# Kernel optimization log

Hardware: AMD Instinct MI355X
Metric: run time of the kernel (lower is better)

Reference implementation:

```python
import jax, jax.numpy as jnp
import numpy as np

N = 50000
E = 800000
D = 256   # output_channel_dim
K = 32
L = 4     # num_of_layers


def setup_inputs() -> dict:
    key = jax.random.key(0)
    ks = jax.random.split(key, 10)
    x = jax.random.normal(ks[0], (N, 1), dtype=jnp.float32)
    edge_index = jax.random.randint(ks[1], (2, E), 0, N, dtype=jnp.int64)
    edge_attr = jax.random.uniform(ks[2], (E,), dtype=jnp.float32)
    # GGNN per-layer propagation weights (L, D, D)
    weight = jax.random.normal(ks[3], (L, D, D), dtype=jnp.float32) / np.sqrt(D)
    # GRUCell params (torch layout: [r|z|n] stacked along first dim)
    w_ih = jax.random.normal(ks[4], (3 * D, D), dtype=jnp.float32) / np.sqrt(D)
    w_hh = jax.random.normal(ks[5], (3 * D, D), dtype=jnp.float32) / np.sqrt(D)
    b_ih = jax.random.normal(ks[6], (3 * D,), dtype=jnp.float32) * 0.01
    b_hh = jax.random.normal(ks[7], (3 * D,), dtype=jnp.float32) * 0.01
    # readout Linear(D, K)
    w_ro = jax.random.normal(ks[8], (D, K), dtype=jnp.float32) / np.sqrt(D)
    b_ro = jax.random.normal(ks[9], (K,), dtype=jnp.float32) * 0.01
    return {"x": x, "edge_index": edge_index, "edge_attr": edge_attr,
            "weight": weight, "w_ih": w_ih, "w_hh": w_hh,
            "b_ih": b_ih, "b_hh": b_hh, "w_ro": w_ro, "b_ro": b_ro}


def _gru_cell(m, h, w_ih, w_hh, b_ih, b_hh):
    # torch.nn.GRUCell math; gates stacked [r|z|n]
    gi = m @ w_ih.T + b_ih   # (N, 3D)
    gh = h @ w_hh.T + b_hh   # (N, 3D)
    i_r, i_z, i_n = jnp.split(gi, 3, axis=-1)
    h_r, h_z, h_n = jnp.split(gh, 3, axis=-1)
    r = jax.nn.sigmoid(i_r + h_r)
    z = jax.nn.sigmoid(i_z + h_z)
    n = jnp.tanh(i_n + r * h_n)
    return (1.0 - z) * n + z * h


def reference(x, edge_index, edge_attr, weight, w_ih, w_hh, b_ih, b_hh, w_ro, b_ro):
    src, dst = edge_index[0], edge_index[1]
    n_nodes, d = x.shape[0], weight.shape[-1]
    # pad input features with zeros up to out_channels
    h = jnp.concatenate([x, jnp.zeros((n_nodes, d - x.shape[-1]), x.dtype)], axis=-1)
    for i in range(weight.shape[0]):
        m = h @ weight[i]                                    # (N, D)
        msg = edge_attr[:, None] * m[src]                    # (E, D)
        agg = jax.ops.segment_sum(msg, dst, num_segments=n_nodes)  # (N, D)
        h = _gru_cell(agg, h, w_ih, w_hh, b_ih, b_hh)
    logits = h @ w_ro + b_ro                                 # (N, K)
    return jax.nn.softmax(logits, axis=-1)
```

## Files before the change

kernel.cpp:

```cpp
#include <hip/hip_runtime.h>

#define D 256
#define K_OUT 32
#define L_LAYERS 4
#define NPAD 50048

typedef __attribute__((ext_vector_type(8))) short bf16x8;
typedef __attribute__((ext_vector_type(4))) float f32x4;
typedef __attribute__((address_space(3))) unsigned int lds_u32;
typedef const __attribute__((address_space(1))) unsigned int glb_u32;

__device__ __forceinline__ float sigm(float v) { return 1.f / (1.f + __expf(-v)); }
__device__ __forceinline__ unsigned short f2bf(float f) {
    unsigned u = __float_as_uint(f);
    u = u + 0x7fffu + ((u >> 16) & 1u);
    return (unsigned short)(u >> 16);
}
__device__ __forceinline__ float bf2f(unsigned short s) {
    return __uint_as_float(((unsigned)s) << 16);
}
__device__ __forceinline__ void gload16(const unsigned short* g, unsigned short* l) {
    __builtin_amdgcn_global_load_lds((glb_u32*)g, (lds_u32*)l, 16, 0, 0);
}

__global__ __launch_bounds__(256) void hist_kernel(const int* __restrict__ dst,
                                                   int* __restrict__ cnt, int E) {
    int idx = blockIdx.x * blockDim.x + threadIdx.x;
    for (int e = idx; e < E; e += gridDim.x * blockDim.x)
        atomicAdd(&cnt[dst[e]], 1);
}

__global__ __launch_bounds__(1024) void scan_kernel(const int* __restrict__ cnt,
                                                    int* __restrict__ rowptr,
                                                    int* __restrict__ cursor, int n) {
    __shared__ int sdata[1024];
    int t = threadIdx.x;
    int chunk = (n + 1023) / 1024;
    int start = t * chunk;
    int end = start + chunk; if (end > n) end = n;
    int s = 0;
    for (int i = start; i < end; i++) s += cnt[i];
    sdata[t] = s;
    __syncthreads();
    for (int off = 1; off < 1024; off <<= 1) {
        int v = (t >= off) ? sdata[t - off] : 0;
        __syncthreads();
        sdata[t] += v;
        __syncthreads();
    }
    int base = sdata[t] - s;
    for (int i = start; i < end; i++) {
        rowptr[i] = base;
        cursor[i] = base;
        base += cnt[i];
    }
    if (end == n && start <= n) rowptr[n] = base;
}

__global__ __launch_bounds__(256) void reorder_kernel(const int* __restrict__ src,
                                                      const int* __restrict__ dst,
                                                      const float* __restrict__ ea,
                                                      int* __restrict__ cursor,
                                                      int* __restrict__ esrc,
                                                      float* __restrict__ eval, int E) {
    int idx = blockIdx.x * blockDim.x + threadIdx.x;
    for (int e = idx; e < E; e += gridDim.x * blockDim.x) {
        int slot = atomicAdd(&cursor[dst[e]], 1);
        esrc[slot] = src[e];
        eval[slot] = ea[e];
    }
}

__global__ __launch_bounds__(256) void prep_wih_kernel(const float* __restrict__ weight,
                                                       const float* __restrict__ w_ih,
                                                       float* __restrict__ P) {
    int l = blockIdx.z;
    const float* A = weight + (size_t)l * D * D;
    float* Cdst = P + (size_t)l * 256 * 768;
    __shared__ float As[32][64 + 4];
    __shared__ float Bs[32][64 + 4];
    int tid = threadIdx.x;
    int tx = tid & 15, ty = tid >> 4;
    int bk = blockIdx.x * 64;
    int bn = blockIdx.y * 64;
    float acc[4][4] = {};
    for (int jb = 0; jb < D; jb += 32) {
        #pragma unroll
        for (int i = 0; i < 2; i++) {
            int lin = tid + i * 256;
            int row = lin >> 3;
            int c4 = (lin & 7) << 2;
            float4 v = *(const float4*)&A[(size_t)(bk + row) * D + jb + c4];
            As[c4+0][row]=v.x; As[c4+1][row]=v.y; As[c4+2][row]=v.z; As[c4+3][row]=v.w;
            float4 w = *(const float4*)&w_ih[(size_t)(bn + row) * D + jb + c4];
            Bs[c4+0][row]=w.x; Bs[c4+1][row]=w.y; Bs[c4+2][row]=w.z; Bs[c4+3][row]=w.w;
        }
        __syncthreads();
        #pragma unroll
        for (int jj = 0; jj < 32; jj++) {
            float a[4], b[4];
            *(float4*)a = *(const float4*)&As[jj][ty*4];
            *(float4*)b = *(const float4*)&Bs[jj][tx*4];
            #pragma unroll
            for (int i = 0; i < 4; i++)
                #pragma unroll
                for (int j = 0; j < 4; j++)
                    acc[i][j] += a[i] * b[j];
        }
        __syncthreads();
    }
    #pragma unroll
    for (int i = 0; i < 4; i++)
        *(float4*)&Cdst[(size_t)(bk + ty*4 + i) * 768 + bn + tx*4] =
            make_float4(acc[i][0], acc[i][1], acc[i][2], acc[i][3]);
}

__global__ __launch_bounds__(256) void pack_bt2_kernel(const float* __restrict__ P,
                                                       const float* __restrict__ w_hh,
                                                       unsigned short* __restrict__ BT2) {
    long long idx = (long long)blockIdx.x * 256 + threadIdx.x;
    int l = (int)(idx >> 20);
    int rem = (int)(idx & 1048575);
    int c = rem >> 10;
    int k2 = rem & 1023;
    int g = c >> 8, d = c & 255;
    int k = k2 & 511;
    float val;
    if (k < 256) {
        val = (g == 0) ? P[(size_t)l * 196608 + (size_t)k * 768 + d]
            : (g == 1) ? P[(size_t)l * 196608 + (size_t)k * 768 + 256 + d]
            : (g == 2) ? P[(size_t)l * 196608 + (size_t)k * 768 + 512 + d]
            : 0.f;
    } else {
        int kk = k - 256;
        val = (g == 0) ? w_hh[(size_t)d * D + kk]
            : (g == 1) ? w_hh[(size_t)(256 + d) * D + kk]
            : (g == 3) ? w_hh[(size_t)(512 + d) * D + kk]
            : 0.f;
    }
    unsigned short hi = f2bf(val);
    BT2[idx] = (k2 < 512) ? hi : f2bf(val - bf2f(hi));
}

__global__ __launch_bounds__(256) void sgather_kernel(const float* __restrict__ x,
                                                      const int* __restrict__ rowptr,
                                                      const int* __restrict__ esrc,
                                                      const float* __restrict__ eval,
                                                      float* __restrict__ sx, int n) {
    int node = blockIdx.x * blockDim.x + threadIdx.x;
    if (node >= n) return;
    float s = 0.f;
    int end = rowptr[node + 1];
    for (int e = rowptr[node]; e < end; e++) s += eval[e] * x[esrc[e]];
    sx[node] = s;
}

__global__ __launch_bounds__(256) void layer0_kernel(const float* __restrict__ x,
                                                     const float* __restrict__ sx,
                                                     const float* __restrict__ P0,
                                                     const float* __restrict__ w_hh,
                                                     const float* __restrict__ b_ih,
                                                     const float* __restrict__ b_hh,
                                                     float* __restrict__ hout, int M) {
    int node = blockIdx.x * 4 + (threadIdx.x >> 6);
    if (node >= M) return;
    int d0 = (threadIdx.x & 63) * 4;
    float sxn = sx[node], xn = x[node];
    float4 r0 = *(const float4*)&P0[d0];
    float4 z0 = *(const float4*)&P0[256 + d0];
    float4 n0 = *(const float4*)&P0[512 + d0];
    float r1[4], z1[4], n1[4];
    #pragma unroll
    for (int j = 0; j < 4; j++) {
        r1[j] = w_hh[(size_t)(d0 + j) * D];
        z1[j] = w_hh[(size_t)(256 + d0 + j) * D];
        n1[j] = w_hh[(size_t)(512 + d0 + j) * D];
    }
    float4 bir = *(const float4*)&b_ih[d0];
    float4 biz = *(const float4*)&b_ih[256 + d0];
    float4 bin = *(const float4*)&b_ih[512 + d0];
    float4 bhr = *(const float4*)&b_hh[d0];
    float4 bhz = *(const float4*)&b_hh[256 + d0];
    float4 bhn = *(const float4*)&b_hh[512 + d0];
    float rr[4] = {sxn*r0.x + xn*r1[0] + bir.x + bhr.x, sxn*r0.y + xn*r1[1] + bir.y + bhr.y,
                   sxn*r0.z + xn*r1[2] + bir.z + bhr.z, sxn*r0.w + xn*r1[3] + bir.w + bhr.w};
    float zz[4] = {sxn*z0.x + xn*z1[0] + biz.x + bhz.x, sxn*z0.y + xn*z1[1] + biz.y + bhz.y,
                   sxn*z0.z + xn*z1[2] + biz.z + bhz.z, sxn*z0.w + xn*z1[3] + biz.w + bhz.w};
    float ni[4] = {sxn*n0.x + bin.x, sxn*n0.y + bin.y, sxn*n0.z + bin.z, sxn*n0.w + bin.w};
    float nh[4] = {xn*n1[0] + bhn.x, xn*n1[1] + bhn.y, xn*n1[2] + bhn.z, xn*n1[3] + bhn.w};
    float o[4];
    #pragma unroll
    for (int j = 0; j < 4; j++) {
        float r = sigm(rr[j]);
        float z = sigm(zz[j]);
        float nn = tanhf(ni[j] + r * nh[j]);
        float hp = (d0 + j == 0) ? xn : 0.f;
        o[j] = (1.f - z) * nn + z * hp;
    }
    *(float4*)&hout[(size_t)node * D + d0] = make_float4(o[0], o[1], o[2], o[3]);
}

__global__ __launch_bounds__(256) void gather_bf_kernel(const float* __restrict__ h,
                                                        const int* __restrict__ rowptr,
                                                        const int* __restrict__ esrc,
                                                        const float* __restrict__ eval,
                                                        unsigned short* __restrict__ A2, int n) {
    int node = (blockIdx.x * 256 + threadIdx.x) >> 6;
    int lane = threadIdx.x & 63;
    if (node >= n) return;
    int beg = rowptr[node], end = rowptr[node + 1];
    float4 acc = make_float4(0.f, 0.f, 0.f, 0.f);
    for (int e = beg; e < end; e++) {
        int s = esrc[e];
        float a = eval[e];
        float4 v = *(const float4*)&h[(size_t)s * D + lane * 4];
        acc.x += a * v.x; acc.y += a * v.y; acc.z += a * v.z; acc.w += a * v.w;
    }
    ushort4 hi = make_ushort4(f2bf(acc.x), f2bf(acc.y), f2bf(acc.z), f2bf(acc.w));
    ushort4 lo = make_ushort4(f2bf(acc.x - bf2f(hi.x)), f2bf(acc.y - bf2f(hi.y)),
                              f2bf(acc.z - bf2f(hi.z)), f2bf(acc.w - bf2f(hi.w)));
    *(ushort4*)&A2[(size_t)node * 1024 + lane * 4] = hi;
    *(ushort4*)&A2[(size_t)node * 1024 + 512 + lane * 4] = lo;
    float4 hv = *(const float4*)&h[(size_t)node * D + lane * 4];
    ushort4 hh = make_ushort4(f2bf(hv.x), f2bf(hv.y), f2bf(hv.z), f2bf(hv.w));
    ushort4 hl = make_ushort4(f2bf(hv.x - bf2f(hh.x)), f2bf(hv.y - bf2f(hh.y)),
                              f2bf(hv.z - bf2f(hh.z)), f2bf(hv.w - bf2f(hh.w)));
    *(ushort4*)&A2[(size_t)node * 1024 + 256 + lane * 4] = hh;
    *(ushort4*)&A2[(size_t)node * 1024 + 768 + lane * 4] = hl;
}

__global__ __launch_bounds__(256, 2) void gru_mfma_kernel(const unsigned short* __restrict__ A2,
                                                          const unsigned short* __restrict__ BT2,
                                                          const float* __restrict__ b_ih,
                                                          const float* __restrict__ b_hh,
                                                          float* __restrict__ h, int M) {
    __shared__ unsigned short sm[2][20480];
    int tid = threadIdx.x;
    int lane = tid & 63;
    int wid = tid >> 6;
    int wr = wid >> 1, wc = wid & 1;
    int bm = blockIdx.x * 128;
    int bnd = blockIdx.y * 64;

    unsigned gbase[10];
    bool gA[10], gG2[10];
    #pragma unroll
    for (int ff = 0; ff < 10; ff++) {
        int f = wid * 10 + ff;
        unsigned row, cb;
        bool isA, isG2 = false;
        if (f < 8)       { row = bm + f * 16 + (lane & 15);        cb = 0;   isA = true; }
        else if (f < 16) { row = bm + (f - 8) * 16 + (lane & 15);  cb = 512; isA = true; }
        else if (f < 28) { int q = f - 16; int gs = q >> 2; int df = q & 3;
                           row = gs * 256 + bnd + df * 16 + (lane & 15); cb = 0; isA = false; isG2 = (gs == 2); }
        else             { int q = f - 28; int gs = q >> 2; int df = q & 3;
                           row = gs * 256 + bnd + df * 16 + (lane & 15); cb = 512; isA = false; isG2 = (gs == 2); }
        gbase[ff] = row * 1024u + cb + ((lane >> 4) << 3);
        gA[ff] = isA; gG2[ff] = isG2;
    }

    f32x4 acc[4][8];
    #pragma unroll
    for (int i = 0; i < 4; i++)
        #pragma unroll
        for (int j = 0; j < 8; j++)
            acc[i][j] = (f32x4){0.f, 0.f, 0.f, 0.f};

#define STAGE(C_, B_)                                                              \
    {                                                                              \
        _Pragma("unroll")                                                          \
        for (int ff = 0; ff < 10; ff++) {                                          \
            const unsigned short* gp = (gA[ff] ? A2 : BT2) + gbase[ff]             \
                + (C_) * 32 + ((gG2[ff] && (C_) >= 8) ? 262144u : 0u);             \
            gload16(gp, &sm[B_][(wid * 10 + ff) * 512]);                           \
        }                                                                          \
    }

#define KBODY(C_, NIOFF_)                                                          \
    {                                                                              \
        int cur = (C_) & 1;                                                        \
        if ((C_) < 15) STAGE((C_) + 1, cur ^ 1);                                   \
        bf16x8 ah[4], al[4], bh[6], bl[6];                                         \
        _Pragma("unroll")                                                          \
        for (int m = 0; m < 4; m++) {                                              \
            ah[m] = *(const bf16x8*)&sm[cur][(wr * 4 + m) * 512 + lane * 8];       \
            al[m] = *(const bf16x8*)&sm[cur][(8 + wr * 4 + m) * 512 + lane * 8];   \
        }                                                                          \
        _Pragma("unroll")                                                          \
        for (int j = 0; j < 6; j++) {                                              \
            int fb = 16 + (j >> 1) * 4 + wc * 2 + (j & 1);                         \
            bh[j] = *(const bf16x8*)&sm[cur][fb * 512 + lane * 8];                 \
            bl[j] = *(const bf16x8*)&sm[cur][(fb + 12) * 512 + lane * 8];          \
        }                                                                          \
        _Pragma("unroll")                                                          \
        for (int m = 0; m < 4; m++) {                                              \
            _Pragma("unroll")                                                      \
            for (int j = 0; j < 6; j++) {                                          \
                int na = (j < 4) ? j : (NIOFF_) + (j & 1);                         \
                acc[m][na] = __builtin_amdgcn_mfma_f32_16x16x32_bf16(ah[m], bh[j], acc[m][na], 0, 0, 0); \
                acc[m][na] = __builtin_amdgcn_mfma_f32_16x16x32_bf16(al[m], bh[j], acc[m][na], 0, 0, 0); \
                acc[m][na] = __builtin_amdgcn_mfma_f32_16x16x32_bf16(ah[m], bl[j], acc[m][na], 0, 0, 0); \
            }                                                                      \
        }                                                                          \
        __syncthreads();                                                           \
    }

    STAGE(0, 0);
    __syncthreads();
    #pragma unroll
    for (int cc = 0; cc < 8; cc++) KBODY(cc, 4)
    #pragma unroll
    for (int cc = 8; cc < 16; cc++) KBODY(cc, 6)
#undef STAGE
#undef KBODY

    int rbase = bm + wr * 64 + ((lane >> 4) << 2);
    #pragma unroll
    for (int jj = 0; jj < 2; jj++) {
        int d = bnd + (wc * 2 + jj) * 16 + (lane & 15);
        float cbr = b_ih[d] + b_hh[d];
        float cbz = b_ih[D + d] + b_hh[D + d];
        float bin = b_ih[2 * D + d];
        float bhn = b_hh[2 * D + d];
        #pragma unroll
        for (int m = 0; m < 4; m++) {
            #pragma unroll
            for (int q = 0; q < 4; q++) {
                int row = rbase + m * 16 + q;
                if (row < M) {
                    float r = sigm(acc[m][jj][q] + cbr);
                    float z = sigm(acc[m][2 + jj][q] + cbz);
                    float nn = tanhf(acc[m][4 + jj][q] + bin + r * (acc[m][6 + jj][q] + bhn));
                    float* hp = &h[(size_t)row * D + d];
                    float hv = *hp;
                    *hp = (1.f - z) * nn + z * hv;
                }
            }
        }
    }
}

__global__ __launch_bounds__(256) void readout_kernel(const float* __restrict__ h,
                                                      const float* __restrict__ w_ro,
                                                      const float* __restrict__ b_ro,
                                                      float* __restrict__ out, int M) {
    __shared__ float ws_[D * K_OUT];
    for (int i = threadIdx.x; i < D * K_OUT; i += 256) ws_[i] = w_ro[i];
    __syncthreads();
    int group = threadIdx.x >> 5;
    int col   = threadIdx.x & 31;
    int node  = blockIdx.x * 8 + group;
    if (node >= M) return;
    float acc = b_ro[col];
    const float* hrow = &h[(size_t)node * D];
    #pragma unroll 8
    for (int k = 0; k < D; k++) acc += hrow[k] * ws_[k * K_OUT + col];
    float mx = acc;
    #pragma unroll
    for (int off = 16; off > 0; off >>= 1) mx = fmaxf(mx, __shfl_xor(mx, off, 32));
    float e = __expf(acc - mx);
    float s = e;
    #pragma unroll
    for (int off = 16; off > 0; off >>= 1) s += __shfl_xor(s, off, 32);
    out[(size_t)node * K_OUT + col] = e / s;
}

extern "C" void kernel_launch(void* const* d_in, const int* in_sizes, int n_in,
                              void* d_out, int out_size, void* d_ws, size_t ws_size,
                              hipStream_t stream) {
    const float* x      = (const float*)d_in[0];
    const int*   ei     = (const int*)d_in[1];
    const float* ea     = (const float*)d_in[2];
    const float* weight = (const float*)d_in[3];
    const float* w_ih   = (const float*)d_in[4];
    const float* w_hh   = (const float*)d_in[5];
    const float* b_ih   = (const float*)d_in[6];
    const float* b_hh   = (const float*)d_in[7];
    const float* w_ro   = (const float*)d_in[8];
    const float* b_ro   = (const float*)d_in[9];
    float* out = (float*)d_out;

    int N = in_sizes[0];
    int E = in_sizes[2];
    const int* src = ei;
    const int* dst = ei + E;

    size_t ND = (size_t)N * D;
    float* h = (float*)d_ws;
    unsigned short* A2 = (unsigned short*)(h + ND);
    float* P = (float*)(A2 + (size_t)NPAD * 1024);
    unsigned short* BT2 = (unsigned short*)(P + (size_t)L_LAYERS * 256 * 768);
    float* sx = (float*)(BT2 + (size_t)L_LAYERS * 1024 * 1024);
    int* cnt = (int*)(sx + N);
    int* rowptr = cnt + (N + 1);
    int* cursor = rowptr + (N + 1);
    int* esrc = cursor + (N + 1);
    float* eval = (float*)(esrc + E);

    hipMemsetAsync(cnt, 0, (N + 1) * sizeof(int), stream);
    hist_kernel<<<1024, 256, 0, stream>>>(dst, cnt, E);
    scan_kernel<<<1, 1024, 0, stream>>>(cnt, rowptr, cursor, N);
    reorder_kernel<<<1024, 256, 0, stream>>>(src, dst, ea, cursor, esrc, eval, E);

    prep_wih_kernel<<<dim3(4, 12, 4), 256, 0, stream>>>(weight, w_ih, P);
    pack_bt2_kernel<<<16384, 256, 0, stream>>>(P, w_hh, BT2);

    sgather_kernel<<<(N + 255) / 256, 256, 0, stream>>>(x, rowptr, esrc, eval, sx, N);
    layer0_kernel<<<(N + 3) / 4, 256, 0, stream>>>(x, sx, P, w_hh, b_ih, b_hh, h, N);

    dim3 gm(NPAD / 128, 4);
    int gather_blocks = (N * 64 + 255) / 256;
    for (int l = 1; l < L_LAYERS; l++) {
        gather_bf_kernel<<<gather_blocks, 256, 0, stream>>>(h, rowptr, esrc, eval, A2, N);
        gru_mfma_kernel<<<gm, 256, 0, stream>>>(A2, BT2 + (size_t)l * 1024 * 1024,
                                                b_ih, b_hh, h, N);
    }
    readout_kernel<<<(N + 7) / 8, 256, 0, stream>>>(h, w_ro, b_ro, out, N);
}
```

Measured before the change: 1.478 ms.

## Split GRU GEMM stage loads into halves with fine-grained waits and swizzle blocks

The GRU MFMA kernel's per-stage global-to-LDS loads are reordered so the hi fragments land first. The kernel now waits on partial vmcnt counts, so the hi*hi MFMAs can start before the lo fragments arrive. Block indices are remapped to a 1D grid where groups of 8 row tiles share each column tile, aiming for better L2 reuse of A2 rows. The readout kernel now loads h as float4 into four independent accumulators to shorten the dependency chain. The manual waitcnt and barrier ordering rely on exact load counts and are fragile if the compiler reorders memory operations.

```diff
diff --git a/kernel.cpp b/kernel.cpp
--- a/kernel.cpp
+++ b/kernel.cpp
@@ -21,6 +21,25 @@
 }
 __device__ __forceinline__ void gload16(const unsigned short* g, unsigned short* l) {
     __builtin_amdgcn_global_load_lds((glb_u32*)g, (lds_u32*)l, 16, 0, 0);
+}
+
+__device__ __forceinline__ void frag_addr(int f, int bm, int bnd, int lane,
+                                          unsigned& off, bool& isA, bool& isG2) {
+    if (f < 8) {
+        off = (unsigned)(bm + f * 16 + (lane & 15)) * 1024u + ((lane >> 4) << 3);
+        isA = true; isG2 = false;
+    } else if (f < 16) {
+        off = (unsigned)(bm + (f - 8) * 16 + (lane & 15)) * 1024u + 512u + ((lane >> 4) << 3);
+        isA = true; isG2 = false;
+    } else if (f < 28) {
+        int q = f - 16; int gs = q >> 2; int df = q & 3;
+        off = (unsigned)(gs * 256 + bnd + df * 16 + (lane & 15)) * 1024u + ((lane >> 4) << 3);
+        isA = false; isG2 = (gs == 2);
+    } else {
+        int q = f - 28; int gs = q >> 2; int df = q & 3;
+        off = (unsigned)(gs * 256 + bnd + df * 16 + (lane & 15)) * 1024u + 512u + ((lane >> 4) << 3);
+        isA = false; isG2 = (gs == 2);
+    }
 }
 
 __global__ __launch_bounds__(256) void hist_kernel(const int* __restrict__ dst,
@@ -239,24 +258,33 @@
     int lane = tid & 63;
     int wid = tid >> 6;
     int wr = wid >> 1, wc = wid & 1;
-    int bm = blockIdx.x * 128;
-    int bnd = blockIdx.y * 64;
-
-    unsigned gbase[10];
-    bool gA[10], gG2[10];
-    #pragma unroll
-    for (int ff = 0; ff < 10; ff++) {
-        int f = wid * 10 + ff;
-        unsigned row, cb;
-        bool isA, isG2 = false;
-        if (f < 8)       { row = bm + f * 16 + (lane & 15);        cb = 0;   isA = true; }
-        else if (f < 16) { row = bm + (f - 8) * 16 + (lane & 15);  cb = 512; isA = true; }
-        else if (f < 28) { int q = f - 16; int gs = q >> 2; int df = q & 3;
-                           row = gs * 256 + bnd + df * 16 + (lane & 15); cb = 0; isA = false; isG2 = (gs == 2); }
-        else             { int q = f - 28; int gs = q >> 2; int df = q & 3;
-                           row = gs * 256 + bnd + df * 16 + (lane & 15); cb = 512; isA = false; isG2 = (gs == 2); }
-        gbase[ff] = row * 1024u + cb + ((lane >> 4) << 3);
-        gA[ff] = isA; gG2[ff] = isG2;
+
+    int bid = blockIdx.x;
+    int g, by;
+    if (bid < 1536) {
+        int ch = bid >> 5;
+        int rem = bid & 31;
+        g = ch * 8 + (rem & 7);
+        by = rem >> 3;
+    } else {
+        int r = bid - 1536;
+        g = 384 + (r >> 2);
+        by = r & 3;
+    }
+    int bm = g * 128;
+    int bnd = by * 64;
+
+    unsigned g0off[5], g1off[5];
+    int slot0[5], slot1[5];
+    bool g0A[5], g0G2[5], g1A[5], g1G2[5];
+    #pragma unroll
+    for (int i = 0; i < 5; i++) {
+        int idx = wid * 5 + i;
+        int f0 = (idx < 8) ? idx : idx + 8;
+        int f1 = (idx < 8) ? idx + 8 : idx + 20;
+        frag_addr(f0, bm, bnd, lane, g0off[i], g0A[i], g0G2[i]);
+        frag_addr(f1, bm, bnd, lane, g1off[i], g1A[i], g1G2[i]);
+        slot0[i] = f0; slot1[i] = f1;
     }
 
     f32x4 acc[4][8];
@@ -266,52 +294,73 @@
         for (int j = 0; j < 8; j++)
             acc[i][j] = (f32x4){0.f, 0.f, 0.f, 0.f};
 
-#define STAGE(C_, B_)                                                              \
-    {                                                                              \
-        _Pragma("unroll")                                                          \
-        for (int ff = 0; ff < 10; ff++) {                                          \
-            const unsigned short* gp = (gA[ff] ? A2 : BT2) + gbase[ff]             \
-                + (C_) * 32 + ((gG2[ff] && (C_) >= 8) ? 262144u : 0u);             \
-            gload16(gp, &sm[B_][(wid * 10 + ff) * 512]);                           \
-        }                                                                          \
-    }
+    bf16x8 ah[4], al[4], bh[6], bl[6];
+
+#define STAGE_H0(C_, B_)                                                           \
+    { _Pragma("unroll")                                                            \
+      for (int i = 0; i < 5; i++) {                                                \
+        const unsigned short* gp = (g0A[i] ? A2 : BT2) + g0off[i]                  \
+            + (C_) * 32 + ((g0G2[i] && (C_) >= 8) ? 262144u : 0u);                 \
+        gload16(gp, &sm[B_][slot0[i] * 512]);                                      \
+      } }
+#define STAGE_H1(C_, B_)                                                           \
+    { _Pragma("unroll")                                                            \
+      for (int i = 0; i < 5; i++) {                                                \
+        const unsigned short* gp = (g1A[i] ? A2 : BT2) + g1off[i]                  \
+            + (C_) * 32 + ((g1G2[i] && (C_) >= 8) ? 262144u : 0u);                 \
+        gload16(gp, &sm[B_][slot1[i] * 512]);                                      \
+      } }
 
 #define KBODY(C_, NIOFF_)                                                          \
-    {                                                                              \
-        int cur = (C_) & 1;                                                        \
-        if ((C_) < 15) STAGE((C_) + 1, cur ^ 1);                                   \
-        bf16x8 ah[4], al[4], bh[6], bl[6];                                         \
-        _Pragma("unroll")                                                          \
-        for (int m = 0; m < 4; m++) {                                              \
+    {   int cur = (C_) & 1;                                                        \
+        asm volatile("s_waitcnt vmcnt(5)" ::: "memory");                           \
+        __builtin_amdgcn_sched_barrier(0);                                         \
+        __builtin_amdgcn_s_barrier();                                              \
+        if ((C_) < 15) { STAGE_H0((C_) + 1, cur ^ 1); STAGE_H1((C_) + 1, cur ^ 1); } \
+        _Pragma("unroll")                                                          \
+        for (int m = 0; m < 4; m++)                                                \
             ah[m] = *(const bf16x8*)&sm[cur][(wr * 4 + m) * 512 + lane * 8];       \
-            al[m] = *(const bf16x8*)&sm[cur][(8 + wr * 4 + m) * 512 + lane * 8];   \
-        }                                                                          \
         _Pragma("unroll")                                                          \
         for (int j = 0; j < 6; j++) {                                              \
             int fb = 16 + (j >> 1) * 4 + wc * 2 + (j & 1);                         \
             bh[j] = *(const bf16x8*)&sm[cur][fb * 512 + lane * 8];                 \
-            bl[j] = *(const bf16x8*)&sm[cur][(fb + 12) * 512 + lane * 8];          \
         }                                                                          \
         _Pragma("unroll")                                                          \
-        for (int m = 0; m < 4; m++) {                                              \
+        for (int m = 0; m < 4; m++)                                                \
             _Pragma("unroll")                                                      \
             for (int j = 0; j < 6; j++) {                                          \
                 int na = (j < 4) ? j : (NIOFF_) + (j & 1);                         \
                 acc[m][na] = __builtin_amdgcn_mfma_f32_16x16x32_bf16(ah[m], bh[j], acc[m][na], 0, 0, 0); \
+            }                                                                      \
+        if ((C_) < 15) { asm volatile("s_waitcnt vmcnt(10)" ::: "memory"); }       \
+        else           { asm volatile("s_waitcnt vmcnt(0)"  ::: "memory"); }       \
+        __builtin_amdgcn_sched_barrier(0);                                         \
+        __builtin_amdgcn_s_barrier();                                              \
+        _Pragma("unroll")                                                          \
+        for (int m = 0; m < 4; m++)                                                \
+            al[m] = *(const bf16x8*)&sm[cur][(8 + wr * 4 + m) * 512 + lane * 8];   \
+        _Pragma("unroll")                                                          \
+        for (int j = 0; j < 6; j++) {                                              \
+            int fb = 16 + (j >> 1) * 4 + wc * 2 + (j & 1);                         \
+            bl[j] = *(const bf16x8*)&sm[cur][(fb + 12) * 512 + lane * 8];          \
+        }                                                                          \
+        _Pragma("unroll")                                                          \
+        for (int m = 0; m < 4; m++)                                                \
+            _Pragma("unroll")                                                      \
+            for (int j = 0; j < 6; j++) {                                          \
+                int na = (j < 4) ? j : (NIOFF_) + (j & 1);                         \
                 acc[m][na] = __builtin_amdgcn_mfma_f32_16x16x32_bf16(al[m], bh[j], acc[m][na], 0, 0, 0); \
                 acc[m][na] = __builtin_amdgcn_mfma_f32_16x16x32_bf16(ah[m], bl[j], acc[m][na], 0, 0, 0); \
             }                                                                      \
-        }                                                                          \
-        __syncthreads();                                                           \
-    }
-
-    STAGE(0, 0);
-    __syncthreads();
-    #pragma unroll
-    for (int cc = 0; cc < 8; cc++) KBODY(cc, 4)
-    #pragma unroll
-    for (int cc = 8; cc < 16; cc++) KBODY(cc, 6)
-#undef STAGE
+    }
+
+    STAGE_H0(0, 0); STAGE_H1(0, 0);
+    KBODY(0, 4)  KBODY(1, 4)  KBODY(2, 4)  KBODY(3, 4)
+    KBODY(4, 4)  KBODY(5, 4)  KBODY(6, 4)  KBODY(7, 4)
+    KBODY(8, 6)  KBODY(9, 6)  KBODY(10, 6) KBODY(11, 6)
+    KBODY(12, 6) KBODY(13, 6) KBODY(14, 6) KBODY(15, 6)
+#undef STAGE_H0
+#undef STAGE_H1
 #undef KBODY
 
     int rbase = bm + wr * 64 + ((lane >> 4) << 2);
@@ -351,10 +400,17 @@
     int col   = threadIdx.x & 31;
     int node  = blockIdx.x * 8 + group;
     if (node >= M) return;
-    float acc = b_ro[col];
+    float a0 = b_ro[col], a1 = 0.f, a2 = 0.f, a3 = 0.f;
     const float* hrow = &h[(size_t)node * D];
-    #pragma unroll 8
-    for (int k = 0; k < D; k++) acc += hrow[k] * ws_[k * K_OUT + col];
+    #pragma unroll 4
+    for (int k = 0; k < D; k += 4) {
+        float4 hv = *(const float4*)&hrow[k];
+        a0 += hv.x * ws_[(k + 0) * K_OUT + col];
+        a1 += hv.y * ws_[(k + 1) * K_OUT + col];
+        a2 += hv.z * ws_[(k + 2) * K_OUT + col];
+        a3 += hv.w * ws_[(k + 3) * K_OUT + col];
+    }
+    float acc = (a0 + a1) + (a2 + a3);
     float mx = acc;
     #pragma unroll
     for (int off = 16; off > 0; off >>= 1) mx = fmaxf(mx, __shfl_xor(mx, off, 32));
@@ -408,11 +464,11 @@
     sgather_kernel<<<(N + 255) / 256, 256, 0, stream>>>(x, rowptr, esrc, eval, sx, N);
     layer0_kernel<<<(N + 3) / 4, 256, 0, stream>>>(x, sx, P, w_hh, b_ih, b_hh, h, N);
 
-    dim3 gm(NPAD / 128, 4);
+    int nb = (NPAD / 128) * 4;
     int gather_blocks = (N * 64 + 255) / 256;
     for (int l = 1; l < L_LAYERS; l++) {
         gather_bf_kernel<<<gather_blocks, 256, 0, stream>>>(h, rowptr, esrc, eval, A2, N);
-        gru_mfma_kernel<<<gm, 256, 0, stream>>>(A2, BT2 + (size_t)l * 1024 * 1024,
+        gru_mfma_kernel<<<nb, 256, 0, stream>>>(A2, BT2 + (size_t)l * 1024 * 1024,
                                                 b_ih, b_hh, h, N);
     }
     readout_kernel<<<(N + 7) / 8, 256, 0, stream>>>(h, w_ro, b_ro, out, N);
```

Result: faster. 1.411 ms (-4.5%).
